# Kernel optimization log

Measured on AMD Instinct MI355X. Metric: run time of the kernel, lower is better.

Reference implementation:

```python
import jax, jax.numpy as jnp
import numpy as np

DROPOUT_P = 0.1


def setup_inputs() -> dict:
    key = jax.random.key(0)
    kq, kk, kv, km = jax.random.split(key, 4)
    B, H, S, D = 8, 16, 1024, 64
    query = jax.random.normal(kq, (B, H, S, D), dtype=jnp.float32)
    key_t = jax.random.normal(kk, (B, H, S, D), dtype=jnp.float32)
    value = jax.random.normal(kv, (B, H, S, D), dtype=jnp.float32)
    mask = jax.random.randint(km, (B, 1, S, S), 0, 2, dtype=jnp.int32)
    return {"query": query, "key": key_t, "value": value, "mask": mask}


def reference(query, key, value, mask):
    d_k = query.shape[-1]
    # scores: [B, H, S, S]
    scores = jnp.einsum("bhqd,bhkd->bhqk", query, key) / jnp.sqrt(
        jnp.asarray(d_k, dtype=query.dtype)
    )
    scores = jnp.where(mask == 0, jnp.asarray(-jnp.inf, dtype=scores.dtype), scores)
    attn_weights = jax.nn.softmax(scores, axis=-1)
    # deterministic dropout (train-mode semantics, fixed RNG)
    drop_key = jax.random.fold_in(jax.random.key(42), 7)
    keep = jax.random.bernoulli(drop_key, 1.0 - DROPOUT_P, attn_weights.shape)
    attn_weights = jnp.where(keep, attn_weights / (1.0 - DROPOUT_P), 0.0)
    output = jnp.einsum("bhqk,bhkd->bhqd", attn_weights, value)
    return (output, attn_weights)
```

## Files before the change

### kernel.cpp

```cpp
#include <hip/hip_runtime.h>


constexpr int Bc = 8, Hc = 16, Sc = 1024, Dc = 64;
constexpr int TQ  = 8;
constexpr int WTP = 12;

typedef float v4f __attribute__((ext_vector_type(4)));

#define TF_ROUND(x0, x1, r) { x0 += x1; x1 = ((x1 << (r)) | (x1 >> (32 - (r)))); x1 ^= x0; }

__host__ __device__ __forceinline__ void threefry2x32(unsigned k0, unsigned k1,
                                                      unsigned x0, unsigned x1,
                                                      unsigned& o0, unsigned& o1) {
  const unsigned k2 = k0 ^ k1 ^ 0x1BD11BDAu;
  x0 += k0; x1 += k1;
  TF_ROUND(x0, x1, 13) TF_ROUND(x0, x1, 15) TF_ROUND(x0, x1, 26) TF_ROUND(x0, x1, 6)
  x0 += k1; x1 += k2 + 1u;
  TF_ROUND(x0, x1, 17) TF_ROUND(x0, x1, 29) TF_ROUND(x0, x1, 16) TF_ROUND(x0, x1, 24)
  x0 += k2; x1 += k0 + 2u;
  TF_ROUND(x0, x1, 13) TF_ROUND(x0, x1, 15) TF_ROUND(x0, x1, 26) TF_ROUND(x0, x1, 6)
  x0 += k0; x1 += k1 + 3u;
  TF_ROUND(x0, x1, 17) TF_ROUND(x0, x1, 29) TF_ROUND(x0, x1, 16) TF_ROUND(x0, x1, 24)
  x0 += k1; x1 += k2 + 4u;
  TF_ROUND(x0, x1, 13) TF_ROUND(x0, x1, 15) TF_ROUND(x0, x1, 26) TF_ROUND(x0, x1, 6)
  x0 += k2; x1 += k0 + 5u;
  o0 = x0; o1 = x1;
}

__global__ __launch_bounds__(256, 3)
void attn_fused(const float* __restrict__ Qg, const float* __restrict__ Kg,
                const float* __restrict__ Vg, const int* __restrict__ Mg,
                float* __restrict__ Og, float* __restrict__ Ag,
                unsigned key0, unsigned key1)
{
  __shared__ __align__(16) float WT[Sc][WTP];
  __shared__ float REDm[4][8];
  __shared__ float REDs[4][8];

  const unsigned orig = blockIdx.x;
  const unsigned wg   = (orig & 7u) * 2048u + (orig >> 3);
  const int q0 = (int)(wg & 127u) * TQ;
  const int h  = (int)(wg >> 7) & 15;
  const int b  = (int)(wg >> 11);

  const int tid = threadIdx.x;
  const int w   = tid >> 6;
  const int l   = tid & 63;
  const size_t bh = (size_t)b * Hc + h;

  const float* __restrict__ Kb = Kg + bh * Sc * Dc;
  const float* __restrict__ Vb = Vg + bh * Sc * Dc;
  const float* __restrict__ Qb = Qg + bh * Sc * Dc + (size_t)q0 * Dc;

  unsigned mbits = 0u;
  {
    const int* __restrict__ mc = Mg + (size_t)b * Sc * Sc + (size_t)q0 * Sc + tid;
    #pragma unroll
    for (int kb = 0; kb < 4; ++kb)
      #pragma unroll
      for (int q = 0; q < 8; ++q)
        mbits |= (mc[(size_t)q * Sc + kb * 256] != 0) ? (1u << (kb * 8 + q)) : 0u;
  }

  unsigned keep = 0u;
  const unsigned ibase = ((unsigned)((b * Hc + h) * Sc + q0)) * (unsigned)Sc
                         + (unsigned)tid;
  #pragma unroll 8
  for (int t2 = 0; t2 < 32; ++t2) {
    const int kb = t2 >> 3, q = t2 & 7;
    unsigned o0, o1;
    threefry2x32(key0, key1, 0u, ibase + (unsigned)(q * Sc + kb * 256), o0, o1);
    const unsigned bits = o0 ^ o1;
    const float u = __uint_as_float((bits >> 9) | 0x3f800000u) - 1.0f;
    keep |= (u < 0.9f) ? (1u << t2) : 0u;
  }

  #pragma unroll 1
  for (int kb = 0; kb < 4; ++kb) {
    const int k = kb * 256 + tid;
    const float4* __restrict__ Krow = (const float4*)(Kb + (size_t)k * Dc);
    float4 kr[16];
    #pragma unroll
    for (int j = 0; j < 16; ++j) kr[j] = Krow[j];
    float acc[8];
    #pragma unroll
    for (int q = 0; q < 8; ++q) {
      const float4* __restrict__ Qrow = (const float4*)(Qb + (size_t)q * Dc);
      float a = 0.f;
      #pragma unroll
      for (int j = 0; j < 16; ++j) {
        const float4 qv = Qrow[j];
        a = fmaf(kr[j].x, qv.x, a);
        a = fmaf(kr[j].y, qv.y, a);
        a = fmaf(kr[j].z, qv.z, a);
        a = fmaf(kr[j].w, qv.w, a);
      }
      acc[q] = a * 0.125f;
    }
    *(float4*)&WT[k][0] = make_float4(acc[0], acc[1], acc[2], acc[3]);
    *(float4*)&WT[k][4] = make_float4(acc[4], acc[5], acc[6], acc[7]);
  }

  const float NEG = -__builtin_inff();
  float sv[4][8];
  #pragma unroll
  for (int kb = 0; kb < 4; ++kb) {
    const int k = kb * 256 + tid;
    const float4 lo = *(const float4*)&WT[k][0];
    const float4 hi = *(const float4*)&WT[k][4];
    sv[kb][0] = lo.x; sv[kb][1] = lo.y; sv[kb][2] = lo.z; sv[kb][3] = lo.w;
    sv[kb][4] = hi.x; sv[kb][5] = hi.y; sv[kb][6] = hi.z; sv[kb][7] = hi.w;
    #pragma unroll
    for (int q = 0; q < 8; ++q)
      if (!((mbits >> (kb * 8 + q)) & 1u)) sv[kb][q] = NEG;
  }

  float mx[8];
  #pragma unroll
  for (int q = 0; q < 8; ++q) {
    float m = fmaxf(fmaxf(sv[0][q], sv[1][q]), fmaxf(sv[2][q], sv[3][q]));
    #pragma unroll
    for (int off = 32; off > 0; off >>= 1) m = fmaxf(m, __shfl_xor(m, off));
    if (l == 0) REDm[w][q] = m;
  }
  __syncthreads();
  #pragma unroll
  for (int q = 0; q < 8; ++q)
    mx[q] = fmaxf(fmaxf(REDm[0][q], REDm[1][q]), fmaxf(REDm[2][q], REDm[3][q]));

  #pragma unroll
  for (int kb = 0; kb < 4; ++kb)
    #pragma unroll
    for (int q = 0; q < 8; ++q)
      sv[kb][q] = __expf(sv[kb][q] - mx[q]);
  #pragma unroll
  for (int q = 0; q < 8; ++q) {
    float s = (sv[0][q] + sv[1][q]) + (sv[2][q] + sv[3][q]);
    #pragma unroll
    for (int off = 32; off > 0; off >>= 1) s += __shfl_xor(s, off);
    if (l == 0) REDs[w][q] = s;
  }
  __syncthreads();
  float inv9[8];
  #pragma unroll
  for (int q = 0; q < 8; ++q)
    inv9[q] = 1.0f / (((REDs[0][q] + REDs[1][q]) + (REDs[2][q] + REDs[3][q])) * 0.9f);

  float* __restrict__ Arow = Ag + bh * (size_t)Sc * Sc + (size_t)q0 * Sc + tid;
  #pragma unroll
  for (int kb = 0; kb < 4; ++kb) {
    const int k = kb * 256 + tid;
    float wv[8];
    #pragma unroll
    for (int q = 0; q < 8; ++q) {
      wv[q] = ((keep >> (kb * 8 + q)) & 1u) ? sv[kb][q] * inv9[q] : 0.f;
      __builtin_nontemporal_store(wv[q], &Arow[(size_t)q * Sc + kb * 256]);
    }
    *(float4*)&WT[k][0] = make_float4(wv[0], wv[1], wv[2], wv[3]);
    *(float4*)&WT[k][4] = make_float4(wv[4], wv[5], wv[6], wv[7]);
  }
  __syncthreads();

  const int ks = tid & 15;
  const int dq = tid >> 4;
  float4 acc[8];
  #pragma unroll
  for (int q = 0; q < 8; ++q) acc[q] = make_float4(0.f, 0.f, 0.f, 0.f);

  #pragma unroll 4
  for (int i = 0; i < 64; ++i) {
    const int k = i * 16 + ks;
    const float4 vv = *(const float4*)(Vb + (size_t)k * Dc + dq * 4);
    const float4 lo = *(const float4*)&WT[k][0];
    const float4 hi = *(const float4*)&WT[k][4];
#define ACCQ(qi, wq) { acc[qi].x = fmaf(wq, vv.x, acc[qi].x); \
                       acc[qi].y = fmaf(wq, vv.y, acc[qi].y); \
                       acc[qi].z = fmaf(wq, vv.z, acc[qi].z); \
                       acc[qi].w = fmaf(wq, vv.w, acc[qi].w); }
    ACCQ(0, lo.x) ACCQ(1, lo.y) ACCQ(2, lo.z) ACCQ(3, lo.w)
    ACCQ(4, hi.x) ACCQ(5, hi.y) ACCQ(6, hi.z) ACCQ(7, hi.w)
#undef ACCQ
  }

  #pragma unroll
  for (int off = 1; off <= 8; off <<= 1) {
    #pragma unroll
    for (int q = 0; q < 8; ++q) {
      acc[q].x += __shfl_xor(acc[q].x, off);
      acc[q].y += __shfl_xor(acc[q].y, off);
      acc[q].z += __shfl_xor(acc[q].z, off);
      acc[q].w += __shfl_xor(acc[q].w, off);
    }
  }
  if ((l & 15) == 0) {
    float* __restrict__ Obase = Og + bh * (size_t)Sc * Dc + (size_t)q0 * Dc + dq * 4;
    #pragma unroll
    for (int q = 0; q < 8; ++q) {
      const v4f t = { acc[q].x, acc[q].y, acc[q].z, acc[q].w };
      __builtin_nontemporal_store(t, (v4f*)(Obase + (size_t)q * Dc));
    }
  }
}

extern "C" void kernel_launch(void* const* d_in, const int* in_sizes, int n_in,
                              void* d_out, int out_size, void* d_ws, size_t ws_size,
                              hipStream_t stream) {
  const float* Qg = (const float*)d_in[0];
  const float* Kg = (const float*)d_in[1];
  const float* Vg = (const float*)d_in[2];
  const int*   Mg = (const int*)d_in[3];
  float* Og = (float*)d_out;
  float* Ag = Og + (size_t)Bc * Hc * Sc * Dc;

  unsigned k0, k1;
  threefry2x32(0u, 42u, 0u, 7u, k0, k1);

  attn_fused<<<dim3(16384), 256, 0, stream>>>(Qg, Kg, Vg, Mg, Og, Ag, k0, k1);
}
```

Measured before the change: 1.720 ms.

## Interchange QK loop to share Q loads across four key rows in registers

Restructures the QK^T score computation so each thread walks the head dimension once and accumulates scores for all four of its key rows at the same time. Each Q float4 load is now reused across four keys instead of one, and the round trip through shared memory (write scores to WT, then read them back) is dropped because the scores stay in registers. The cost is higher register pressure from 32 live accumulators plus four K vectors, which could hurt occupancy under the 3-blocks-per-SM launch bound. The four K loads per step are strided by the row length rather than forming a contiguous 256-byte row.

```diff
diff --git a/kernel.cpp b/kernel.cpp
--- a/kernel.cpp
+++ b/kernel.cpp
@@ -75,45 +75,54 @@
     keep |= (u < 0.9f) ? (1u << t2) : 0u;
   }
 
-  #pragma unroll 1
-  for (int kb = 0; kb < 4; ++kb) {
-    const int k = kb * 256 + tid;
-    const float4* __restrict__ Krow = (const float4*)(Kb + (size_t)k * Dc);
-    float4 kr[16];
-    #pragma unroll
-    for (int j = 0; j < 16; ++j) kr[j] = Krow[j];
-    float acc[8];
-    #pragma unroll
-    for (int q = 0; q < 8; ++q) {
-      const float4* __restrict__ Qrow = (const float4*)(Qb + (size_t)q * Dc);
-      float a = 0.f;
+  float sv[4][8];
+  #pragma unroll
+  for (int c = 0; c < 4; ++c)
+    #pragma unroll
+    for (int q = 0; q < 8; ++q) sv[c][q] = 0.f;
+
+  {
+    const float4* __restrict__ Kp0 = (const float4*)(Kb + (size_t)(      tid) * Dc);
+    const float4* __restrict__ Kp1 = (const float4*)(Kb + (size_t)(256 + tid) * Dc);
+    const float4* __restrict__ Kp2 = (const float4*)(Kb + (size_t)(512 + tid) * Dc);
+    const float4* __restrict__ Kp3 = (const float4*)(Kb + (size_t)(768 + tid) * Dc);
+    #pragma unroll 1
+    for (int j = 0; j < 16; ++j) {
+      const float4 kv0 = Kp0[j];
+      const float4 kv1 = Kp1[j];
+      const float4 kv2 = Kp2[j];
+      const float4 kv3 = Kp3[j];
       #pragma unroll
-      for (int j = 0; j < 16; ++j) {
-        const float4 qv = Qrow[j];
-        a = fmaf(kr[j].x, qv.x, a);
-        a = fmaf(kr[j].y, qv.y, a);
-        a = fmaf(kr[j].z, qv.z, a);
-        a = fmaf(kr[j].w, qv.w, a);
+      for (int q = 0; q < 8; ++q) {
+        const float4 qv = *(const float4*)(Qb + (size_t)q * Dc + j * 4);
+        sv[0][q] = fmaf(kv0.x, qv.x, sv[0][q]);
+        sv[0][q] = fmaf(kv0.y, qv.y, sv[0][q]);
+        sv[0][q] = fmaf(kv0.z, qv.z, sv[0][q]);
+        sv[0][q] = fmaf(kv0.w, qv.w, sv[0][q]);
+        sv[1][q] = fmaf(kv1.x, qv.x, sv[1][q]);
+        sv[1][q] = fmaf(kv1.y, qv.y, sv[1][q]);
+        sv[1][q] = fmaf(kv1.z, qv.z, sv[1][q]);
+        sv[1][q] = fmaf(kv1.w, qv.w, sv[1][q]);
+        sv[2][q] = fmaf(kv2.x, qv.x, sv[2][q]);
+        sv[2][q] = fmaf(kv2.y, qv.y, sv[2][q]);
+        sv[2][q] = fmaf(kv2.z, qv.z, sv[2][q]);
+        sv[2][q] = fmaf(kv2.w, qv.w, sv[2][q]);
+        sv[3][q] = fmaf(kv3.x, qv.x, sv[3][q]);
+        sv[3][q] = fmaf(kv3.y, qv.y, sv[3][q]);
+        sv[3][q] = fmaf(kv3.z, qv.z, sv[3][q]);
+        sv[3][q] = fmaf(kv3.w, qv.w, sv[3][q]);
       }
-      acc[q] = a * 0.125f;
-    }
-    *(float4*)&WT[k][0] = make_float4(acc[0], acc[1], acc[2], acc[3]);
-    *(float4*)&WT[k][4] = make_float4(acc[4], acc[5], acc[6], acc[7]);
+    }
   }
 
   const float NEG = -__builtin_inff();
-  float sv[4][8];
-  #pragma unroll
-  for (int kb = 0; kb < 4; ++kb) {
-    const int k = kb * 256 + tid;
-    const float4 lo = *(const float4*)&WT[k][0];
-    const float4 hi = *(const float4*)&WT[k][4];
-    sv[kb][0] = lo.x; sv[kb][1] = lo.y; sv[kb][2] = lo.z; sv[kb][3] = lo.w;
-    sv[kb][4] = hi.x; sv[kb][5] = hi.y; sv[kb][6] = hi.z; sv[kb][7] = hi.w;
-    #pragma unroll
-    for (int q = 0; q < 8; ++q)
-      if (!((mbits >> (kb * 8 + q)) & 1u)) sv[kb][q] = NEG;
-  }
+  #pragma unroll
+  for (int kb = 0; kb < 4; ++kb)
+    #pragma unroll
+    for (int q = 0; q < 8; ++q) {
+      const float s = sv[kb][q] * 0.125f;
+      sv[kb][q] = ((mbits >> (kb * 8 + q)) & 1u) ? s : NEG;
+    }
 
   float mx[8];
   #pragma unroll
```

Result: slower. 1.908 ms (+11.0%).
